# Kernel tuning notes

Measured on AMD Instinct MI355X. Metric: run time of the kernel, lower is better.

## Reference

```python
import jax, jax.numpy as jnp
import numpy as np

B, S, H, HEADS = 4, 2048, 512, 8
DK = H // HEADS
LN_EPS = 1e-5
NEG_INF = -1e30


def setup_inputs() -> dict:
    key = jax.random.key(0)
    k = jax.random.split(key, 6)
    x = jax.random.normal(k[0], (B, S, H), dtype=jnp.float32)
    mask = jax.random.randint(k[1], (B, S), 0, 2, dtype=jnp.int32)
    # per-head Q/K/V projection weights stacked: [heads, H, dk]
    Wq = jax.random.normal(k[2], (HEADS, H, DK), dtype=jnp.float32) * 0.05
    Wk = jax.random.normal(k[3], (HEADS, H, DK), dtype=jnp.float32) * 0.05
    Wv = jax.random.normal(k[4], (HEADS, H, DK), dtype=jnp.float32) * 0.05
    # output projection: [heads*dk, H] (y = h @ Wo)
    Wo = jax.random.normal(k[5], (HEADS * DK, H), dtype=jnp.float32) * 0.05
    gamma = jnp.ones((H,), dtype=jnp.float32)
    beta = jnp.zeros((H,), dtype=jnp.float32)
    return {"x": x, "mask": mask, "Wq": Wq, "Wk": Wk, "Wv": Wv,
            "Wo": Wo, "gamma": gamma, "beta": beta}


def reference(x, mask, Wq, Wk, Wv, Wo, gamma, beta):
    # LayerNorm over hidden dim
    mu = jnp.mean(x, axis=-1, keepdims=True)
    var = jnp.mean(jnp.square(x - mu), axis=-1, keepdims=True)
    xn = (x - mu) * jax.lax.rsqrt(var + LN_EPS) * gamma + beta  # [B,S,H]

    mf = mask.astype(jnp.float32)  # [B,S]

    # batched per-head projections (original loops over heads)
    q = jnp.einsum('bsh,nhd->bnsd', xn, Wq)  # [B,heads,S,dk]
    kk = jnp.einsum('bsh,nhd->bnsd', xn, Wk)
    v = jnp.einsum('bsh,nhd->bnsd', xn, Wv)

    scores = jnp.einsum('bnqd,bnkd->bnqk', q, kk) / np.sqrt(DK).astype(np.float32)
    m = mf[:, None, None, :]  # [B,1,1,S] broadcast over query dim
    logits = m * scores + (1.0 - m) * NEG_INF
    probs = jax.nn.softmax(logits, axis=-1)
    attn = jnp.einsum('bnqk,bnkd->bnqd', probs, v)  # [B,heads,S,dk]

    h = attn.transpose(0, 2, 1, 3).reshape(x.shape[0], x.shape[1], HEADS * DK)
    out = h @ Wo + xn          # residual adds post-norm x (as in original)
    out = out * mf[:, :, None]  # zero out masked positions
    return out
```

## Files before the change

### kernel.cpp

```cpp
#include <hip/hip_runtime.h>
#include <hip/hip_bf16.h>
#include <math.h>

#define B_ 4
#define S_ 2048
#define H_ 512
#define HEADS_ 8
#define DK_ 64
#define NROWS_ (B_*S_)
#define LN_EPS_ 1e-5f
#define NEG_INF_ -1e30f
#define QSCALE_ (0.125f * 1.44269504088896f)

typedef short s8v __attribute__((ext_vector_type(8)));
typedef short s4v __attribute__((ext_vector_type(4)));
typedef float f4v __attribute__((ext_vector_type(4)));

typedef __attribute__((address_space(1))) unsigned int gu32_t;
typedef __attribute__((address_space(3))) unsigned int lu32_t;

__device__ __forceinline__ unsigned short f2bf(float f) {
    unsigned int u = __float_as_uint(f);
    u += 0x7FFFu + ((u >> 16) & 1u);
    return (unsigned short)(u >> 16);
}

__device__ __forceinline__ float bf2f(unsigned short u) {
    return __uint_as_float((unsigned int)u << 16);
}

__device__ __forceinline__ s4v pk4bf(float a, float b, float c, float d) {
    union { __hip_bfloat162 h[2]; s4v v; } u;
    u.h[0] = __float22bfloat162_rn(float2{a, b});
    u.h[1] = __float22bfloat162_rn(float2{c, d});
    return u.v;
}

__global__ __launch_bounds__(256) void prep_kernel(
        const float* __restrict__ x, const float* __restrict__ gamma,
        const float* __restrict__ beta, const int* __restrict__ mask,
        const float* __restrict__ Wq, const float* __restrict__ Wk,
        const float* __restrict__ Wv, const float* __restrict__ Wo,
        unsigned short* __restrict__ xnb, float* __restrict__ mb,
        unsigned short* __restrict__ Wt) {
    int bx = blockIdx.x;
    if (bx < 2048) {
        int row  = bx * 4 + (threadIdx.x >> 6);
        int lane = threadIdx.x & 63;
        const float4* xr = (const float4*)(x + (size_t)row * H_ + lane * 8);
        float4 a = xr[0], d = xr[1];
        float s  = (a.x + a.y) + (a.z + a.w) + (d.x + d.y) + (d.z + d.w);
        float ss = (a.x*a.x + a.y*a.y) + (a.z*a.z + a.w*a.w)
                 + (d.x*d.x + d.y*d.y) + (d.z*d.z + d.w*d.w);
        #pragma unroll
        for (int i = 1; i < 64; i <<= 1) {
            s  += __shfl_xor(s, i, 64);
            ss += __shfl_xor(ss, i, 64);
        }
        float mu  = s * (1.f / 512.f);
        float var = ss * (1.f / 512.f) - mu * mu;
        float rstd = rsqrtf(var + LN_EPS_);
        if (lane == 0) mb[row] = mask[row] ? 0.f : NEG_INF_;
        const float4* gp = (const float4*)(gamma + lane * 8);
        const float4* bp = (const float4*)(beta + lane * 8);
        float4 g0 = gp[0], g1 = gp[1], b0 = bp[0], b1 = bp[1];
        float4 y0, y1;
        y0.x = (a.x - mu) * rstd * g0.x + b0.x;
        y0.y = (a.y - mu) * rstd * g0.y + b0.y;
        y0.z = (a.z - mu) * rstd * g0.z + b0.z;
        y0.w = (a.w - mu) * rstd * g0.w + b0.w;
        y1.x = (d.x - mu) * rstd * g1.x + b1.x;
        y1.y = (d.y - mu) * rstd * g1.y + b1.y;
        y1.z = (d.z - mu) * rstd * g1.z + b1.z;
        y1.w = (d.w - mu) * rstd * g1.w + b1.w;
        union { s4v h[2]; s8v v; } pk;
        pk.h[0] = pk4bf(y0.x, y0.y, y0.z, y0.w);
        pk.h[1] = pk4bf(y1.x, y1.y, y1.z, y1.w);
        *(s8v*)(xnb + (size_t)row * H_ + lane * 8) = pk.v;
    } else {
        __shared__ float tile[32][33];
        int wid = bx - 2048;
        const float* src;
        int ld, drow, k0, c0;
        float scale = 1.f;
        if (wid < 768) {
            int z = wid >> 5, rem = wid & 31;
            int cx = rem & 1, ky = rem >> 1;
            k0 = ky * 32; c0 = cx * 32;
            int zw = z >> 3, head = z & 7;
            const float* W = (zw == 0) ? Wq : (zw == 1) ? Wk : Wv;
            if (zw == 0) scale = QSCALE_;
            src = W + (size_t)head * H_ * DK_;
            ld = DK_;
            drow = zw * 512 + head * 64;
        } else {
            int rem = wid - 768;
            int cx = rem & 15, ky = rem >> 4;
            k0 = ky * 32; c0 = cx * 32;
            src = Wo; ld = H_; drow = 1536;
        }
        int tx = threadIdx.x & 31, ty = threadIdx.x >> 5;
        #pragma unroll
        for (int i = 0; i < 4; i++)
            tile[ty * 4 + i][tx] = src[(size_t)(k0 + ty * 4 + i) * ld + c0 + tx];
        __syncthreads();
        #pragma unroll
        for (int i = 0; i < 4; i++) {
            int cc = ty * 4 + i;
            Wt[(size_t)(drow + c0 + cc) * 512 + k0 + tx] = f2bf(tile[tx][cc] * scale);
        }
    }
}

__device__ __forceinline__ void gemm_tile(
        const unsigned short* __restrict__ A,
        const unsigned short* __restrict__ Bt,
        int r0, int j0, f4v acc[4][4]) {
    __shared__ unsigned short As[2 * 128 * 32];
    __shared__ unsigned short Bs[2 * 128 * 32];
    int t = threadIdx.x;
    int wv = t >> 6, L = t & 63, c = L & 15, g = L >> 4;
    int m_base = (wv & 1) * 64, n_base = (wv >> 1) * 64;
    #pragma unroll
    for (int i = 0; i < 4; i++)
        #pragma unroll
        for (int j = 0; j < 4; j++) acc[i][j] = (f4v){0.f, 0.f, 0.f, 0.f};
    for (int k0 = 0; k0 < 512; k0 += 64) {
        __syncthreads();
        #pragma unroll
        for (int half = 0; half < 2; half++) {
            #pragma unroll
            for (int i = 0; i < 2; i++) {
                int u = wv * 128 + i * 64 + L;
                int row = u >> 2, k16 = u & 3;
                __builtin_amdgcn_global_load_lds(
                    (const gu32_t*)(A + (size_t)(r0 + row) * 512 + k0 + half * 32 + k16 * 8),
                    (lu32_t*)(As + half * 4096 + (size_t)(wv * 128 + i * 64) * 8), 16, 0, 0);
                __builtin_amdgcn_global_load_lds(
                    (const gu32_t*)(Bt + (size_t)(j0 + row) * 512 + k0 + half * 32 + k16 * 8),
                    (lu32_t*)(Bs + half * 4096 + (size_t)(wv * 128 + i * 64) * 8), 16, 0, 0);
            }
        }
        __asm__ volatile("s_waitcnt vmcnt(0)" ::: "memory");
        __syncthreads();
        #pragma unroll
        for (int half = 0; half < 2; half++) {
            s8v a[4], b[4];
            #pragma unroll
            for (int i = 0; i < 4; i++)
                a[i] = *(const s8v*)(As + half * 4096 + (size_t)(m_base + i * 16 + c) * 32 + g * 8);
            #pragma unroll
            for (int j = 0; j < 4; j++)
                b[j] = *(const s8v*)(Bs + half * 4096 + (size_t)(n_base + j * 16 + c) * 32 + g * 8);
            #pragma unroll
            for (int i = 0; i < 4; i++)
                #pragma unroll
                for (int j = 0; j < 4; j++)
                    acc[i][j] = __builtin_amdgcn_mfma_f32_16x16x32_bf16(
                        a[i], b[j], acc[i][j], 0, 0, 0);
        }
    }
}

__global__ __launch_bounds__(256) void qkv_gemm(
        const unsigned short* __restrict__ xnb,
        const unsigned short* __restrict__ Wt,
        unsigned short* __restrict__ Qb, unsigned short* __restrict__ Kf,
        unsigned short* __restrict__ Vf) {
    f4v acc[4][4];
    int t = threadIdx.x;
    int wv = t >> 6, L = t & 63, c = L & 15, g = L >> 4;
    int rb = wv & 1, cb = wv >> 1;
    if (blockIdx.x < 8) {
        int m0 = blockIdx.x * 128, n0 = blockIdx.y * 128;
        gemm_tile(Wt, xnb, m0, n0, acc);
        int R0 = m0 + rb * 64;
        int C0 = n0 + cb * 64;
        int hd = (R0 >> 6) & 7;
        int b  = C0 >> 11, srow0 = C0 & 2047;
        size_t bhbase = (size_t)(b * HEADS_ + hd) * S_ * DK_;
        if (R0 < 512) {
            #pragma unroll
            for (int msub = 0; msub < 4; msub++) {
                int dk4 = msub * 16 + g * 4;
                #pragma unroll
                for (int nsub = 0; nsub < 4; nsub++) {
                    int tok = srow0 + nsub * 16 + c;
                    s4v v = pk4bf(acc[msub][nsub][0], acc[msub][nsub][1],
                                  acc[msub][nsub][2], acc[msub][nsub][3]);
                    *(s4v*)(Qb + bhbase + (size_t)tok * DK_ + dk4) = v;
                }
            }
        } else {
            unsigned short* dst = Kf + bhbase + (size_t)(srow0 >> 6) * 4096;
            #pragma unroll
            for (int msub = 0; msub < 4; msub++) {
                int gx = (msub & 1) * 2 + (g >> 1);
                int slotbase = (g & 1) * 4 + (msub >> 1) * 8;
                #pragma unroll
                for (int nsub = 0; nsub < 4; nsub++) {
                    s4v v = pk4bf(acc[msub][nsub][0], acc[msub][nsub][1],
                                  acc[msub][nsub][2], acc[msub][nsub][3]);
                    *(s4v*)(dst + nsub * 1024 + (gx * 16 + c) * 16 + slotbase) = v;
                }
            }
        }
    } else {
        int r0 = blockIdx.y * 128, j0 = 1024 + (blockIdx.x - 8) * 128;
        gemm_tile(xnb, Wt, r0, j0, acc);
        int R0 = r0 + rb * 64;
        int C0 = j0 + cb * 64;
        int hd = (C0 >> 6) & 7;
        int b = R0 >> 11, srow0 = R0 & 2047;
        unsigned short* dst = Vf + (size_t)(b * HEADS_ + hd) * S_ * DK_
                              + (size_t)(srow0 >> 6) * 4096;
        #pragma unroll
        for (int msub = 0; msub < 4; msub++)
            #pragma unroll
            for (int nsub = 0; nsub < 4; nsub++) {
                s4v v = pk4bf(acc[msub][nsub][0], acc[msub][nsub][1],
                              acc[msub][nsub][2], acc[msub][nsub][3]);
                *(s4v*)(dst + nsub * 1024 + (g * 16 + c) * 16 + msub * 4) = v;
            }
    }
}

__global__ __launch_bounds__(256, 3) void attn_kernel(
        const unsigned short* __restrict__ Qb,
        const unsigned short* __restrict__ Kf,
        const unsigned short* __restrict__ Vf,
        const float* __restrict__ mb,
        unsigned short* __restrict__ hb) {
    __shared__ float red[2][64][2][17];

    int wv   = threadIdx.x >> 6;
    int qsub = wv & 1;
    int kp   = wv >> 1;
    int L  = threadIdx.x & 63;
    int c  = L & 15;
    int g  = L >> 4;

    unsigned wgid = blockIdx.x + blockIdx.y * 32u;
    unsigned xcd  = wgid & 7u;
    unsigned idx  = wgid >> 3;
    int bh = (int)(xcd + (idx >> 5) * 8u);
    int qt = (int)(idx & 31u);
    int b  = bh >> 3, n = bh & 7;
    int q0 = qt * 64 + qsub * 32;

    const unsigned short* Qbase = Qb + (size_t)bh * S_ * DK_;
    const unsigned short* Kp = Kf + (size_t)bh * S_ * DK_ + (size_t)kp * 16 * 4096 + L * 16;
    const unsigned short* Vp = Vf + (size_t)bh * S_ * DK_ + (size_t)kp * 16 * 4096 + L * 16;
    const float* mbrow = mb + b * S_ + kp * 1024;

    s8v qfA0 = *(const s8v*)(Qbase + (size_t)(q0 + c) * DK_ + g * 8);
    s8v qfA1 = *(const s8v*)(Qbase + (size_t)(q0 + c) * DK_ + 32 + g * 8);
    s8v qfB0 = *(const s8v*)(Qbase + (size_t)(q0 + 16 + c) * DK_ + g * 8);
    s8v qfB1 = *(const s8v*)(Qbase + (size_t)(q0 + 16 + c) * DK_ + 32 + g * 8);

    f4v accA[4], accB[4];
    #pragma unroll
    for (int i = 0; i < 4; i++) {
        accA[i] = (f4v){0.f, 0.f, 0.f, 0.f};
        accB[i] = (f4v){0.f, 0.f, 0.f, 0.f};
    }
    float lacA[4] = {0.f, 0.f, 0.f, 0.f};
    float lacB[4] = {0.f, 0.f, 0.f, 0.f};

    for (int kb = 0; kb < 16; kb++) {
        const unsigned short* Kn = Kp + (size_t)kb * 4096;
        const unsigned short* Vn = Vp + (size_t)kb * 4096;
        #pragma unroll
        for (int h = 0; h < 2; h++) {
            s8v k0lo = *(const s8v*)(Kn + (h * 2 + 0) * 1024);
            s8v k0hi = *(const s8v*)(Kn + (h * 2 + 0) * 1024 + 8);
            s8v k1lo = *(const s8v*)(Kn + (h * 2 + 1) * 1024);
            s8v k1hi = *(const s8v*)(Kn + (h * 2 + 1) * 1024 + 8);
            float4 mb0 = *(const float4*)(mbrow + kb * 64 + h * 32 + g * 4);
            float4 mb1 = *(const float4*)(mbrow + kb * 64 + h * 32 + 16 + g * 4);
            s8v vv[4];
            #pragma unroll
            for (int ds = 0; ds < 4; ds++)
                vv[ds] = *(const s8v*)(Vn + ds * 1024 + h * 8);
            f4v bias0 = (f4v){mb0.x, mb0.y, mb0.z, mb0.w};
            f4v bias1 = (f4v){mb1.x, mb1.y, mb1.z, mb1.w};
            f4v sA0 = bias0, sA1 = bias1, sB0 = bias0, sB1 = bias1;
            sA0 = __builtin_amdgcn_mfma_f32_16x16x32_bf16(k0lo, qfA0, sA0, 0, 0, 0);
            sA0 = __builtin_amdgcn_mfma_f32_16x16x32_bf16(k0hi, qfA1, sA0, 0, 0, 0);
            sA1 = __builtin_amdgcn_mfma_f32_16x16x32_bf16(k1lo, qfA0, sA1, 0, 0, 0);
            sA1 = __builtin_amdgcn_mfma_f32_16x16x32_bf16(k1hi, qfA1, sA1, 0, 0, 0);
            sB0 = __builtin_amdgcn_mfma_f32_16x16x32_bf16(k0lo, qfB0, sB0, 0, 0, 0);
            sB0 = __builtin_amdgcn_mfma_f32_16x16x32_bf16(k0hi, qfB1, sB0, 0, 0, 0);
            sB1 = __builtin_amdgcn_mfma_f32_16x16x32_bf16(k1lo, qfB0, sB1, 0, 0, 0);
            sB1 = __builtin_amdgcn_mfma_f32_16x16x32_bf16(k1hi, qfB1, sB1, 0, 0, 0);
            float pA0[4], pA1[4], pB0[4], pB1[4];
            #pragma unroll
            for (int r = 0; r < 4; r++) {
                pA0[r] = __builtin_amdgcn_exp2f(sA0[r]);
                pA1[r] = __builtin_amdgcn_exp2f(sA1[r]);
                pB0[r] = __builtin_amdgcn_exp2f(sB0[r]);
                pB1[r] = __builtin_amdgcn_exp2f(sB1[r]);
                lacA[r] += pA0[r] + pA1[r];
                lacB[r] += pB0[r] + pB1[r];
            }
            s4v pfA0 = pk4bf(pA0[0], pA0[1], pA0[2], pA0[3]);
            s4v pfA1 = pk4bf(pA1[0], pA1[1], pA1[2], pA1[3]);
            s4v pfB0 = pk4bf(pB0[0], pB0[1], pB0[2], pB0[3]);
            s4v pfB1 = pk4bf(pB1[0], pB1[1], pB1[2], pB1[3]);
            #pragma unroll
            for (int ds = 0; ds < 4; ds++) {
                s4v v0 = __builtin_shufflevector(vv[ds], vv[ds], 0, 1, 2, 3);
                s4v v1 = __builtin_shufflevector(vv[ds], vv[ds], 4, 5, 6, 7);
                accA[ds] = __builtin_amdgcn_mfma_f32_16x16x16bf16_1k(v0, pfA0, accA[ds], 0, 0, 0);
                accA[ds] = __builtin_amdgcn_mfma_f32_16x16x16bf16_1k(v1, pfA1, accA[ds], 0, 0, 0);
                accB[ds] = __builtin_amdgcn_mfma_f32_16x16x16bf16_1k(v0, pfB0, accB[ds], 0, 0, 0);
                accB[ds] = __builtin_amdgcn_mfma_f32_16x16x16bf16_1k(v1, pfB1, accB[ds], 0, 0, 0);
            }
        }
    }

    float lA = (lacA[0] + lacA[1]) + (lacA[2] + lacA[3]);
    float lB = (lacB[0] + lacB[1]) + (lacB[2] + lacB[3]);
    lA += __shfl_xor(lA, 16, 64);
    lA += __shfl_xor(lA, 32, 64);
    lB += __shfl_xor(lB, 16, 64);
    lB += __shfl_xor(lB, 32, 64);

    if (kp == 1) {
        #pragma unroll
        for (int d = 0; d < 4; d++) {
            #pragma unroll
            for (int r = 0; r < 4; r++) {
                red[qsub][L][0][d * 4 + r] = accA[d][r];
                red[qsub][L][1][d * 4 + r] = accB[d][r];
            }
        }
        red[qsub][L][0][16] = lA;
        red[qsub][L][1][16] = lB;
    }
    __syncthreads();
    if (kp == 0) {
        const float* srcA = &red[qsub][L][0][0];
        const float* srcB = &red[qsub][L][1][0];
        float invA = 1.f / (lA + srcA[16]);
        float invB = 1.f / (lB + srcB[16]);
        unsigned short* hpA = hb + (size_t)(b * S_ + q0 + c) * H_ + n * DK_ + g * 4;
        unsigned short* hpB = hpA + (size_t)16 * H_;
        #pragma unroll
        for (int ds = 0; ds < 4; ds++) {
            s4v oA = pk4bf((accA[ds][0] + srcA[ds * 4 + 0]) * invA,
                           (accA[ds][1] + srcA[ds * 4 + 1]) * invA,
                           (accA[ds][2] + srcA[ds * 4 + 2]) * invA,
                           (accA[ds][3] + srcA[ds * 4 + 3]) * invA);
            *(s4v*)(hpA + ds * 16) = oA;
            s4v oB = pk4bf((accB[ds][0] + srcB[ds * 4 + 0]) * invB,
                           (accB[ds][1] + srcB[ds * 4 + 1]) * invB,
                           (accB[ds][2] + srcB[ds * 4 + 2]) * invB,
                           (accB[ds][3] + srcB[ds * 4 + 3]) * invB);
            *(s4v*)(hpB + ds * 16) = oB;
        }
    }
}

__global__ __launch_bounds__(256) void out_gemm(
        const unsigned short* __restrict__ hb,
        const unsigned short* __restrict__ Wot,
        const unsigned short* __restrict__ xnb, const int* __restrict__ mask,
        float* __restrict__ out) {
    f4v acc[4][4];
    int r0 = blockIdx.y * 128, j0 = blockIdx.x * 128;
    gemm_tile(hb, Wot, r0, j0, acc);
    int t = threadIdx.x;
    int wv = t >> 6, L = t & 63, c = L & 15, g = L >> 4;
    int mrow = r0 + (wv & 1) * 64 + g * 4;
    int ncol = j0 + (wv >> 1) * 64 + c;
    #pragma unroll
    for (int msub = 0; msub < 4; msub++) {
        #pragma unroll
        for (int rr = 0; rr < 4; rr++) {
            int row = mrow + msub * 16 + rr;
            float mf = (float)mask[row];
            #pragma unroll
            for (int nsub = 0; nsub < 4; nsub++) {
                int col = ncol + nsub * 16;
                size_t o = (size_t)row * H_ + col;
                out[o] = (acc[msub][nsub][rr] + bf2f(xnb[o])) * mf;
            }
        }
    }
}

extern "C" void kernel_launch(void* const* d_in, const int* in_sizes, int n_in,
                              void* d_out, int out_size, void* d_ws, size_t ws_size,
                              hipStream_t stream) {
    const float* x     = (const float*)d_in[0];
    const int*   mask  = (const int*)d_in[1];
    const float* Wq    = (const float*)d_in[2];
    const float* Wk    = (const float*)d_in[3];
    const float* Wv    = (const float*)d_in[4];
    const float* Wo    = (const float*)d_in[5];
    const float* gamma = (const float*)d_in[6];
    const float* beta  = (const float*)d_in[7];
    float* out = (float*)d_out;

    size_t nelem = (size_t)NROWS_ * H_;
    char* ws = (char*)d_ws;
    unsigned short* xnb = (unsigned short*)ws; ws += nelem * 2;
    unsigned short* hb  = (unsigned short*)ws; ws += nelem * 2;
    unsigned short* Qb  = (unsigned short*)ws; ws += nelem * 2;
    unsigned short* Kf  = (unsigned short*)ws; ws += nelem * 2;
    unsigned short* Vf  = (unsigned short*)ws; ws += nelem * 2;
    unsigned short* Wt  = (unsigned short*)ws; ws += (size_t)2048 * 512 * 2;
    float*          mbp = (float*)ws;

    prep_kernel<<<3072, 256, 0, stream>>>(
        x, gamma, beta, mask, Wq, Wk, Wv, Wo, xnb, mbp, Wt);
    qkv_gemm<<<dim3(12, 64), 256, 0, stream>>>(xnb, Wt, Qb, Kf, Vf);
    attn_kernel<<<dim3(S_ / 64, B_ * HEADS_), 256, 0, stream>>>(
        Qb, Kf, Vf, mbp, hb);
    out_gemm<<<dim3(4, 64), 256, 0, stream>>>(
        hb, Wt + (size_t)1536 * 512, xnb, mask, out);
}
```

Baseline: 175.5 us.

## Split attention key range across four waves per 32-query block

Each workgroup now handles 32 queries instead of 64, and its four waves each process a quarter of the key sequence instead of two query halves times two key halves. The grid doubles to 2048 workgroups and the XCD-aware block index mapping is adjusted to match. The final reduction merges three partial accumulators and denominators through a larger shared buffer. This shortens each wave's serial key loop and raises parallelism. In exchange, every K/V tile is loaded by twice as many workgroups and the cross-wave reduction does more work.

```diff
diff --git a/kernel.cpp b/kernel.cpp
--- a/kernel.cpp
+++ b/kernel.cpp
@@ -231,27 +231,25 @@
         const unsigned short* __restrict__ Vf,
         const float* __restrict__ mb,
         unsigned short* __restrict__ hb) {
-    __shared__ float red[2][64][2][17];
-
-    int wv   = threadIdx.x >> 6;
-    int qsub = wv & 1;
-    int kp   = wv >> 1;
+    __shared__ float red[3][64][2][17];
+
+    int kp = threadIdx.x >> 6;
     int L  = threadIdx.x & 63;
     int c  = L & 15;
     int g  = L >> 4;
 
-    unsigned wgid = blockIdx.x + blockIdx.y * 32u;
+    unsigned wgid = blockIdx.x + blockIdx.y * 64u;
     unsigned xcd  = wgid & 7u;
     unsigned idx  = wgid >> 3;
-    int bh = (int)(xcd + (idx >> 5) * 8u);
-    int qt = (int)(idx & 31u);
+    int bh = (int)(xcd + (idx >> 6) * 8u);
+    int qt = (int)(idx & 63u);
     int b  = bh >> 3, n = bh & 7;
-    int q0 = qt * 64 + qsub * 32;
+    int q0 = qt * 32;
 
     const unsigned short* Qbase = Qb + (size_t)bh * S_ * DK_;
-    const unsigned short* Kp = Kf + (size_t)bh * S_ * DK_ + (size_t)kp * 16 * 4096 + L * 16;
-    const unsigned short* Vp = Vf + (size_t)bh * S_ * DK_ + (size_t)kp * 16 * 4096 + L * 16;
-    const float* mbrow = mb + b * S_ + kp * 1024;
+    const unsigned short* Kp = Kf + (size_t)bh * S_ * DK_ + (size_t)kp * 8 * 4096 + L * 16;
+    const unsigned short* Vp = Vf + (size_t)bh * S_ * DK_ + (size_t)kp * 8 * 4096 + L * 16;
+    const float* mbrow = mb + b * S_ + kp * 512;
 
     s8v qfA0 = *(const s8v*)(Qbase + (size_t)(q0 + c) * DK_ + g * 8);
     s8v qfA1 = *(const s8v*)(Qbase + (size_t)(q0 + c) * DK_ + 32 + g * 8);
@@ -267,7 +265,7 @@
     float lacA[4] = {0.f, 0.f, 0.f, 0.f};
     float lacB[4] = {0.f, 0.f, 0.f, 0.f};
 
-    for (int kb = 0; kb < 16; kb++) {
+    for (int kb = 0; kb < 8; kb++) {
         const unsigned short* Kn = Kp + (size_t)kb * 4096;
         const unsigned short* Vn = Vp + (size_t)kb * 4096;
         #pragma unroll
@@ -326,37 +324,46 @@
     lB += __shfl_xor(lB, 16, 64);
     lB += __shfl_xor(lB, 32, 64);
 
-    if (kp == 1) {
+    if (kp >= 1) {
         #pragma unroll
         for (int d = 0; d < 4; d++) {
             #pragma unroll
             for (int r = 0; r < 4; r++) {
-                red[qsub][L][0][d * 4 + r] = accA[d][r];
-                red[qsub][L][1][d * 4 + r] = accB[d][r];
-            }
-        }
-        red[qsub][L][0][16] = lA;
-        red[qsub][L][1][16] = lB;
+                red[kp - 1][L][0][d * 4 + r] = accA[d][r];
+                red[kp - 1][L][1][d * 4 + r] = accB[d][r];
+            }
+        }
+        red[kp - 1][L][0][16] = lA;
+        red[kp - 1][L][1][16] = lB;
     }
     __syncthreads();
     if (kp == 0) {
-        const float* srcA = &red[qsub][L][0][0];
-        const float* srcB = &red[qsub][L][1][0];
-        float invA = 1.f / (lA + srcA[16]);
-        float invB = 1.f / (lB + srcB[16]);
+        #pragma unroll
+        for (int w = 0; w < 3; w++) {
+            const float* srcA = &red[w][L][0][0];
+            const float* srcB = &red[w][L][1][0];
+            #pragma unroll
+            for (int d = 0; d < 4; d++) {
+                #pragma unroll
+                for (int r = 0; r < 4; r++) {
+                    accA[d][r] += srcA[d * 4 + r];
+                    accB[d][r] += srcB[d * 4 + r];
+                }
+            }
+            lA += srcA[16];
+            lB += srcB[16];
+        }
+        float invA = 1.f / lA;
+        float invB = 1.f / lB;
         unsigned short* hpA = hb + (size_t)(b * S_ + q0 + c) * H_ + n * DK_ + g * 4;
         unsigned short* hpB = hpA + (size_t)16 * H_;
         #pragma unroll
         for (int ds = 0; ds < 4; ds++) {
-            s4v oA = pk4bf((accA[ds][0] + srcA[ds * 4 + 0]) * invA,
-                           (accA[ds][1] + srcA[ds * 4 + 1]) * invA,
-                           (accA[ds][2] + srcA[ds * 4 + 2]) * invA,
-                           (accA[ds][3] + srcA[ds * 4 + 3]) * invA);
+            s4v oA = pk4bf(accA[ds][0] * invA, accA[ds][1] * invA,
+                           accA[ds][2] * invA, accA[ds][3] * invA);
             *(s4v*)(hpA + ds * 16) = oA;
-            s4v oB = pk4bf((accB[ds][0] + srcB[ds * 4 + 0]) * invB,
-                           (accB[ds][1] + srcB[ds * 4 + 1]) * invB,
-                           (accB[ds][2] + srcB[ds * 4 + 2]) * invB,
-                           (accB[ds][3] + srcB[ds * 4 + 3]) * invB);
+            s4v oB = pk4bf(accB[ds][0] * invB, accB[ds][1] * invB,
+                           accB[ds][2] * invB, accB[ds][3] * invB);
             *(s4v*)(hpB + ds * 16) = oB;
         }
     }
@@ -416,7 +423,7 @@
     prep_kernel<<<3072, 256, 0, stream>>>(
         x, gamma, beta, mask, Wq, Wk, Wv, Wo, xnb, mbp, Wt);
     qkv_gemm<<<dim3(12, 64), 256, 0, stream>>>(xnb, Wt, Qb, Kf, Vf);
-    attn_kernel<<<dim3(S_ / 64, B_ * HEADS_), 256, 0, stream>>>(
+    attn_kernel<<<dim3(S_ / 32, B_ * HEADS_), 256, 0, stream>>>(
         Qb, Kf, Vf, mbp, hb);
     out_gemm<<<dim3(4, 64), 256, 0, stream>>>(
         hb, Wt + (size_t)1536 * 512, xnb, mask, out);
```

Result: slower. 187.6 us (+6.9%).
